# Performance work log

Hardware: AMD Instinct MI355X
Metric: run time of the kernel (lower is better)

The kernel has to match this reference:

```python
import jax, jax.numpy as jnp
import numpy as np

N_TREES = 64
DEPTH = 10           # complete binary trees
ARITY = 2
C = 8                # hidden states
M = 32               # observation labels
G = 8                # n_gen
NPT = 2 ** (DEPTH + 1) - 1   # nodes per tree = 2047
DIM = N_TREES * NPT          # 131008 total nodes


def _levels(parents_cat, children_cat):
    # Static (Python-int) slicing: level d has N_TREES * 2**d children.
    levels, pos = [], 0
    for d in range(1, DEPTH + 1):
        n = N_TREES * (2 ** d)
        levels.append((parents_cat[pos:pos + n], children_cat[pos:pos + n]))
        pos += n
    return levels


def _forward(A, B, Pi, x, roots, leaves, inv_map, trees_ind, parents_cat, children_cat):
    sm_A = jax.nn.softmax(A, axis=0)    # (C,C,G), columns sum to 1 over first axis
    sm_B = jax.nn.softmax(B, axis=1)    # (C,M,G)
    sm_Pi = jax.nn.softmax(Pi, axis=0)  # (C,G)
    log_A, log_Pi = jnp.log(sm_A), jnp.log(sm_Pi)

    levels = _levels(parents_cat, children_cat)
    obs = x[inv_map]
    emit = lambda idx: jnp.transpose(sm_B[:, obs[idx]], (1, 0, 2))  # (n,C,G)

    # ---- preliminary downward: prior[n,i,g] ----
    prior = jnp.zeros((DIM, C, G), dtype=A.dtype)
    prior = prior.at[roots].set(jnp.broadcast_to(sm_Pi, (roots.shape[0], C, G)))
    for pa, ch in levels:
        prior = prior.at[ch].set(jnp.einsum('ijg,njg->nig', sm_A, prior[pa]))

    # ---- upward (beta recursion) ----
    beta = jnp.zeros((DIM, C, G), dtype=A.dtype)
    t_beta = jnp.zeros((DIM, C, G), dtype=A.dtype)
    bl = prior[leaves] * emit(leaves)
    beta = beta.at[leaves].set(bl / bl.sum(1, keepdims=True))
    for pa, ch in reversed(levels):
        ratio = beta[ch] / prior[ch]                       # (n,C,G)
        beta_uv = jnp.einsum('ijg,nig->njg', sm_A, ratio)  # message child->parent
        t_beta = t_beta.at[ch].set(beta_uv)
        u_idx = pa[::ARITY]                                # unique parents (children are contiguous pairs)
        prod_u = beta_uv.reshape(-1, ARITY, C, G).prod(axis=1)  # segmented product over siblings
        bu = prior[u_idx] * emit(u_idx) * prod_u
        beta = beta.at[u_idx].set(bu / bu.sum(1, keepdims=True))

    # ---- downward (eps / t_eps posteriors) ----
    eps = jnp.zeros((DIM, C, G), dtype=A.dtype)
    t_eps = jnp.zeros((DIM, C, C, G), dtype=A.dtype)
    eps = eps.at[roots].set(beta[roots])
    for pa, ch in levels:
        pa_factor = eps[pa][:, None, :, :] * sm_A[None] / t_beta[ch][:, None, :, :]  # (n,C,C,G)
        ch_factor = (beta[ch] / prior[ch])[:, :, None, :]                            # (n,C,1,G)
        te = ch_factor * pa_factor
        t_eps = t_eps.at[ch].set(te)
        num = te.sum(2)
        eps = eps.at[ch].set(num / num.sum(1, keepdims=True))

    # ---- log likelihood, scattered per tree ----
    lik = jnp.zeros((DIM, G), dtype=A.dtype)
    lik = lik.at[roots].add((eps[roots] * log_Pi[None]).sum(1))
    no_root = jnp.concatenate([ch for _, ch in levels])
    lik = lik.at[no_root].add((t_eps[no_root] * log_A[None]).sum((1, 2)))
    internal = jnp.concatenate([pa[::ARITY] for pa, _ in levels])
    all_nodes = jnp.concatenate([internal, leaves])
    lik = lik.at[all_nodes].add((eps[all_nodes] * jnp.log(emit(all_nodes))).sum(1))
    ll = jax.ops.segment_sum(lik, trees_ind, num_segments=N_TREES)  # (N_TREES, G)
    return -ll


def setup_inputs() -> dict:
    key = jax.random.key(0)
    kA, kB, kPi, kx = jax.random.split(key, 4)
    A = jax.random.normal(kA, (C, C, G), dtype=jnp.float32)
    B = jax.random.normal(kB, (C, M, G), dtype=jnp.float32)
    Pi = jax.random.normal(kPi, (C, G), dtype=jnp.float32)
    x = jax.random.randint(kx, (DIM,), 0, M, dtype=jnp.int32)

    offsets = np.arange(N_TREES, dtype=np.int64) * NPT
    parents, children = [], []
    for d in range(1, DEPTH + 1):
        cl = np.arange(2 ** d - 1, 2 ** (d + 1) - 1)   # local child indices at level d
        pl = (cl - 1) // 2                             # local parent indices
        children.append((offsets[:, None] + cl[None, :]).ravel())
        parents.append((offsets[:, None] + pl[None, :]).ravel())
    parents_cat = jnp.asarray(np.concatenate(parents), dtype=jnp.int32)
    children_cat = jnp.asarray(np.concatenate(children), dtype=jnp.int32)
    leaves = jnp.asarray(children[-1], dtype=jnp.int32)
    roots = jnp.asarray(offsets, dtype=jnp.int32)
    inv_map = jnp.arange(DIM, dtype=jnp.int32)
    trees_ind = jnp.asarray(np.repeat(np.arange(N_TREES), NPT), dtype=jnp.int32)
    return {"A": A, "B": B, "Pi": Pi, "x": x, "roots": roots, "leaves": leaves,
            "inv_map": inv_map, "trees_ind": trees_ind,
            "parents_cat": parents_cat, "children_cat": children_cat}


def reference(A, B, Pi, x, roots, leaves, inv_map, trees_ind, parents_cat, children_cat):
    return _forward(A, B, Pi, x, roots, leaves, inv_map, trees_ind, parents_cat, children_cat)
```

## Files before the change

### kernel.cpp

```cpp
#include <hip/hip_runtime.h>


#define NTREES 64
#define DEPTH  10
#define C      8
#define M      32
#define G      8
#define NPT    2047
#define PAD    9
#define BLOCK  512
#define LNODES 1023

__device__ __forceinline__ float frcp(float v) { return __builtin_amdgcn_rcpf(v); }

template<bool WEPS>
__device__ __forceinline__ float child_node(const float (&sA)[C][C],
                                            const float (&sAL)[C][C],
                                            const float (&lgB)[C][M],
                                            const float (&r)[C],
                                            const float (&epa)[C],
                                            int xv,
                                            float (&eout)[C])
{
    float f[C];
    #pragma unroll
    for (int j = 0; j < C; ++j) {
        float tb = 0.f;
        #pragma unroll
        for (int i = 0; i < C; ++i) tb += sA[i][j] * r[i];
        f[j] = epa[j] * frcp(tb);
    }
    float S = 0.f, likA = 0.f, num[C];
    #pragma unroll
    for (int i = 0; i < C; ++i) {
        float a = 0.f, la = 0.f;
        #pragma unroll
        for (int j = 0; j < C; ++j) { a += sA[i][j] * f[j]; la += sAL[i][j] * f[j]; }
        num[i] = r[i] * a;
        S     += num[i];
        likA  += r[i] * la;
    }
    const float invS = frcp(S);
    float likE = 0.f;
    #pragma unroll
    for (int i = 0; i < C; ++i) {
        const float e2 = num[i] * invS;
        if constexpr (WEPS) eout[i] = e2;
        likE += e2 * lgB[i][xv];
    }
    return likA + likE;
}

__global__ __launch_bounds__(BLOCK, 2)
void htmm_kernel(const float* __restrict__ A,
                 const float* __restrict__ B,
                 const float* __restrict__ Pi,
                 const int*   __restrict__ x,
                 float* __restrict__ out)
{
    __shared__ float buf[LNODES * PAD];
    __shared__ float sA[C][C], sAL[C][C];
    __shared__ float sB[C][M], lgB[C][M];
    __shared__ float spi[C],  lgpi[C];
    __shared__ float bls[C];
    __shared__ float red8[BLOCK / 64];

    const int b   = blockIdx.x;
    const int t   = b >> 3;
    const int g   = b & 7;
    const int tid = threadIdx.x;
    const int base = t * NPT;

    if (tid < C) {
        const int j = tid;
        float w[C]; float mx = -1e30f;
        #pragma unroll
        for (int i = 0; i < C; ++i) { w[i] = A[(i*C + j)*G + g]; mx = fmaxf(mx, w[i]); }
        float s = 0.f; float e[C];
        #pragma unroll
        for (int i = 0; i < C; ++i) { e[i] = expf(w[i] - mx); s += e[i]; }
        const float inv = 1.f / s, ls = logf(s);
        #pragma unroll
        for (int i = 0; i < C; ++i) {
            const float sm = e[i] * inv;
            sA[i][j]  = sm;
            sAL[i][j] = sm * ((w[i] - mx) - ls);
        }
    } else if (tid == 8) {
        float w[C]; float mx = -1e30f;
        #pragma unroll
        for (int c = 0; c < C; ++c) { w[c] = Pi[c*G + g]; mx = fmaxf(mx, w[c]); }
        float s = 0.f; float e[C];
        #pragma unroll
        for (int c = 0; c < C; ++c) { e[c] = expf(w[c] - mx); s += e[c]; }
        const float inv = 1.f / s, ls = logf(s);
        #pragma unroll
        for (int c = 0; c < C; ++c) { spi[c] = e[c]*inv; lgpi[c] = (w[c]-mx) - ls; }
    } else if (tid >= 64 && tid < 64 + C) {
        const int c = tid - 64;
        float mx = -1e30f;
        for (int m = 0; m < M; ++m) mx = fmaxf(mx, B[(c*M + m)*G + g]);
        float s = 0.f;
        for (int m = 0; m < M; ++m) s += expf(B[(c*M + m)*G + g] - mx);
        bls[c] = mx + logf(s);
    }
    __syncthreads();

    if (tid < C * M) {
        const int c = tid >> 5, m = tid & 31;
        const float d0 = B[(c*M + m)*G + g] - bls[c];
        lgB[c][m] = d0;
        sB[c][m]  = expf(d0);
    }
    if (tid == 320) {
        #pragma unroll
        for (int i = 0; i < C; ++i) buf[i] = spi[i];
    }
    __syncthreads();

    for (int d = 1; d <= 8; ++d) {
        const int half = 1 << (d - 1);
        if (tid < half) {
            const int u = half - 1 + tid;
            const int cb = 2*u + 1;
            float p[C];
            #pragma unroll
            for (int j = 0; j < C; ++j) p[j] = buf[u*PAD + j];
            #pragma unroll
            for (int i = 0; i < C; ++i) {
                float acc = 0.f;
                #pragma unroll
                for (int j = 0; j < C; ++j) acc += sA[i][j] * p[j];
                buf[cb*PAD + i]       = acc;
                buf[(cb + 1)*PAD + i] = acc;
            }
        }
        __syncthreads();
    }

    const int s  = 511 + tid;
    const int xs = x[base + s];
    const int x1 = x[base + 2*s + 1];
    const int x2 = x[base + 2*s + 2];

    float ps[C], pc[C];
    {
        const int pas = 255 + (tid >> 1);
        float pp[C];
        #pragma unroll
        for (int j = 0; j < C; ++j) pp[j] = buf[pas*PAD + j];
        #pragma unroll
        for (int i = 0; i < C; ++i) {
            float a = 0.f;
            #pragma unroll
            for (int j = 0; j < C; ++j) a += sA[i][j] * pp[j];
            ps[i] = a;
        }
        #pragma unroll
        for (int i = 0; i < C; ++i) {
            float a = 0.f;
            #pragma unroll
            for (int j = 0; j < C; ++j) a += sA[i][j] * ps[j];
            pc[i] = a;
        }
    }

    float rs[C], r1[C], r2[C];
    {
        float Z1 = 0.f, Z2 = 0.f;
        #pragma unroll
        for (int i = 0; i < C; ++i) {
            r1[i] = sB[i][x1]; Z1 += pc[i] * r1[i];
            r2[i] = sB[i][x2]; Z2 += pc[i] * r2[i];
        }
        const float i1 = frcp(Z1), i2 = frcp(Z2);
        #pragma unroll
        for (int i = 0; i < C; ++i) { r1[i] *= i1; r2[i] *= i2; }
        float Z = 0.f;
        #pragma unroll
        for (int j = 0; j < C; ++j) {
            float a1 = 0.f, a2 = 0.f;
            #pragma unroll
            for (int i = 0; i < C; ++i) { a1 += sA[i][j]*r1[i]; a2 += sA[i][j]*r2[i]; }
            rs[j] = sB[j][xs] * (a1 * a2);
            Z += ps[j] * rs[j];
        }
        const float iz = frcp(Z);
        #pragma unroll
        for (int j = 0; j < C; ++j) { rs[j] *= iz; buf[s*PAD + j] = rs[j]; }
    }
    __syncthreads();

    for (int d = 8; d >= 0; --d) {
        if (tid < (1 << d)) {
            const int u = (1 << d) - 1 + tid;
            const int c1 = 2*u + 1;
            float rr1[C], rr2[C];
            #pragma unroll
            for (int i = 0; i < C; ++i) { rr1[i] = buf[c1*PAD + i]; rr2[i] = buf[(c1+1)*PAD + i]; }
            const int xu = x[base + u];
            float pr[C], ep[C]; float Z = 0.f;
            #pragma unroll
            for (int j = 0; j < C; ++j) {
                float a1 = 0.f, a2 = 0.f;
                #pragma unroll
                for (int i = 0; i < C; ++i) { a1 += sA[i][j]*rr1[i]; a2 += sA[i][j]*rr2[i]; }
                ep[j] = sB[j][xu] * (a1 * a2);
                pr[j] = buf[u*PAD + j];
                Z += pr[j] * ep[j];
            }
            const float iz = frcp(Z);
            if (d) {
                #pragma unroll
                for (int j = 0; j < C; ++j) buf[u*PAD + j] = ep[j]*iz;
            } else {
                #pragma unroll
                for (int j = 0; j < C; ++j) buf[j] = pr[j]*ep[j]*iz;
            }
        }
        __syncthreads();
    }

    float lik = 0.f;
    if (tid == 0) {
        const int xr = x[base];
        #pragma unroll
        for (int c = 0; c < C; ++c) lik += buf[c] * (lgpi[c] + lgB[c][xr]);
    }
    for (int d = 1; d <= 8; ++d) {
        if (tid < (1 << d)) {
            const int v = (1 << d) - 1 + tid, pa = (v - 1) >> 1;
            float epa[C], r[C], eo[C];
            #pragma unroll
            for (int j = 0; j < C; ++j) epa[j] = buf[pa*PAD + j];
            #pragma unroll
            for (int i = 0; i < C; ++i) r[i] = buf[v*PAD + i];
            lik += child_node<true>(sA, sAL, lgB, r, epa, x[base + v], eo);
            #pragma unroll
            for (int i = 0; i < C; ++i) buf[v*PAD + i] = eo[i];
        }
        __syncthreads();
    }
    {
        const int pas = 255 + (tid >> 1);
        float epa[C], es[C], dummy[C];
        #pragma unroll
        for (int j = 0; j < C; ++j) epa[j] = buf[pas*PAD + j];
        lik += child_node<true >(sA, sAL, lgB, rs, epa, xs, es);
        lik += child_node<false>(sA, sAL, lgB, r1, es,  x1, dummy);
        lik += child_node<false>(sA, sAL, lgB, r2, es,  x2, dummy);
    }

    #pragma unroll
    for (int off = 32; off; off >>= 1) lik += __shfl_xor(lik, off, 64);
    if ((tid & 63) == 0) red8[tid >> 6] = lik;
    __syncthreads();
    if (tid == 0) {
        float acc = 0.f;
        #pragma unroll
        for (int w = 0; w < BLOCK/64; ++w) acc += red8[w];
        out[t*G + g] = -acc;
    }
}

extern "C" void kernel_launch(void* const* d_in, const int* in_sizes, int n_in,
                              void* d_out, int out_size, void* d_ws, size_t ws_size,
                              hipStream_t stream) {
    const float* A  = (const float*)d_in[0];
    const float* B  = (const float*)d_in[1];
    const float* Pi = (const float*)d_in[2];
    const int*   x  = (const int*)d_in[3];
    float* out = (float*)d_out;
    htmm_kernel<<<NTREES * G, BLOCK, 0, stream>>>(A, B, Pi, x, out);
}
```

Baseline: 117.0 us.

## Process two tree levels per barrier in the down, up and posterior passes

Each thread now handles a node together with its children (or grandchildren) in one step, so the prior, beta and posterior sweeps take about half as many __syncthreads barriers. The aim is to cut the serial barrier-bound level chain in a kernel where most threads sit idle at the upper levels. The cost is redundant work per thread and more live registers. Global loads of x for the leaf frontier are also hoisted ahead of the softmax setup so their latency overlaps it.

```diff
diff --git a/kernel.cpp b/kernel.cpp
--- a/kernel.cpp
+++ b/kernel.cpp
@@ -13,6 +13,54 @@
 
 __device__ __forceinline__ float frcp(float v) { return __builtin_amdgcn_rcpf(v); }
 
+__device__ __forceinline__ void ldsRead(const float* buf, int node, float (&v)[C]) {
+    #pragma unroll
+    for (int i = 0; i < C; ++i) v[i] = buf[node*PAD + i];
+}
+__device__ __forceinline__ void ldsWrite(float* buf, int node, const float (&v)[C]) {
+    #pragma unroll
+    for (int i = 0; i < C; ++i) buf[node*PAD + i] = v[i];
+}
+
+__device__ __forceinline__ void matvec(const float (&sA)[C][C], const float (&p)[C],
+                                       float (&o)[C]) {
+    #pragma unroll
+    for (int i = 0; i < C; ++i) {
+        float a = 0.f;
+        #pragma unroll
+        for (int j = 0; j < C; ++j) a += sA[i][j] * p[j];
+        o[i] = a;
+    }
+}
+
+template<bool ROOT>
+__device__ __forceinline__ void up_node(const float (&sA)[C][C], const float (&sB)[C][M],
+                                        const float (&rr1)[C], const float (&rr2)[C],
+                                        const float (&pr)[C], int xu, float (&outv)[C])
+{
+    float a1[C], a2[C];
+    #pragma unroll
+    for (int j = 0; j < C; ++j) { a1[j] = 0.f; a2[j] = 0.f; }
+    #pragma unroll
+    for (int i = 0; i < C; ++i) {
+        #pragma unroll
+        for (int j = 0; j < C; ++j) {
+            const float aij = sA[i][j];
+            a1[j] += aij * rr1[i];
+            a2[j] += aij * rr2[i];
+        }
+    }
+    float ep[C]; float Z = 0.f;
+    #pragma unroll
+    for (int j = 0; j < C; ++j) {
+        ep[j] = sB[j][xu] * (a1[j] * a2[j]);
+        Z += pr[j] * ep[j];
+    }
+    const float iz = frcp(Z);
+    #pragma unroll
+    for (int j = 0; j < C; ++j) outv[j] = ROOT ? pr[j]*ep[j]*iz : ep[j]*iz;
+}
+
 template<bool WEPS>
 __device__ __forceinline__ float child_node(const float (&sA)[C][C],
                                             const float (&sAL)[C][C],
@@ -22,14 +70,17 @@
                                             int xv,
                                             float (&eout)[C])
 {
+    float tb[C];
+    #pragma unroll
+    for (int j = 0; j < C; ++j) tb[j] = 0.f;
+    #pragma unroll
+    for (int i = 0; i < C; ++i) {
+        #pragma unroll
+        for (int j = 0; j < C; ++j) tb[j] += sA[i][j] * r[i];
+    }
     float f[C];
     #pragma unroll
-    for (int j = 0; j < C; ++j) {
-        float tb = 0.f;
-        #pragma unroll
-        for (int i = 0; i < C; ++i) tb += sA[i][j] * r[i];
-        f[j] = epa[j] * frcp(tb);
-    }
+    for (int j = 0; j < C; ++j) f[j] = epa[j] * frcp(tb[j]);
     float S = 0.f, likA = 0.f, num[C];
     #pragma unroll
     for (int i = 0; i < C; ++i) {
@@ -71,15 +122,20 @@
     const int tid = threadIdx.x;
     const int base = t * NPT;
 
+    const int s  = 511 + tid;
+    const int xs = x[base + s];
+    const int x1 = x[base + 2*s + 1];
+    const int x2 = x[base + 2*s + 2];
+
     if (tid < C) {
         const int j = tid;
         float w[C]; float mx = -1e30f;
         #pragma unroll
         for (int i = 0; i < C; ++i) { w[i] = A[(i*C + j)*G + g]; mx = fmaxf(mx, w[i]); }
-        float s = 0.f; float e[C];
-        #pragma unroll
-        for (int i = 0; i < C; ++i) { e[i] = expf(w[i] - mx); s += e[i]; }
-        const float inv = 1.f / s, ls = logf(s);
+        float s0 = 0.f; float e[C];
+        #pragma unroll
+        for (int i = 0; i < C; ++i) { e[i] = expf(w[i] - mx); s0 += e[i]; }
+        const float inv = 1.f / s0, ls = logf(s0);
         #pragma unroll
         for (int i = 0; i < C; ++i) {
             const float sm = e[i] * inv;
@@ -90,19 +146,21 @@
         float w[C]; float mx = -1e30f;
         #pragma unroll
         for (int c = 0; c < C; ++c) { w[c] = Pi[c*G + g]; mx = fmaxf(mx, w[c]); }
-        float s = 0.f; float e[C];
-        #pragma unroll
-        for (int c = 0; c < C; ++c) { e[c] = expf(w[c] - mx); s += e[c]; }
-        const float inv = 1.f / s, ls = logf(s);
+        float s0 = 0.f; float e[C];
+        #pragma unroll
+        for (int c = 0; c < C; ++c) { e[c] = expf(w[c] - mx); s0 += e[c]; }
+        const float inv = 1.f / s0, ls = logf(s0);
         #pragma unroll
         for (int c = 0; c < C; ++c) { spi[c] = e[c]*inv; lgpi[c] = (w[c]-mx) - ls; }
     } else if (tid >= 64 && tid < 64 + C) {
         const int c = tid - 64;
         float mx = -1e30f;
+        #pragma unroll
         for (int m = 0; m < M; ++m) mx = fmaxf(mx, B[(c*M + m)*G + g]);
-        float s = 0.f;
-        for (int m = 0; m < M; ++m) s += expf(B[(c*M + m)*G + g] - mx);
-        bls[c] = mx + logf(s);
+        float s0 = 0.f;
+        #pragma unroll
+        for (int m = 0; m < M; ++m) s0 += expf(B[(c*M + m)*G + g] - mx);
+        bls[c] = mx + logf(s0);
     }
     __syncthreads();
 
@@ -118,53 +176,30 @@
     }
     __syncthreads();
 
-    for (int d = 1; d <= 8; ++d) {
-        const int half = 1 << (d - 1);
-        if (tid < half) {
-            const int u = half - 1 + tid;
-            const int cb = 2*u + 1;
-            float p[C];
-            #pragma unroll
-            for (int j = 0; j < C; ++j) p[j] = buf[u*PAD + j];
-            #pragma unroll
-            for (int i = 0; i < C; ++i) {
-                float acc = 0.f;
-                #pragma unroll
-                for (int j = 0; j < C; ++j) acc += sA[i][j] * p[j];
-                buf[cb*PAD + i]       = acc;
-                buf[(cb + 1)*PAD + i] = acc;
-            }
+    #pragma unroll 1
+    for (int p = 0; p < 8; p += 2) {
+        if (tid < (1 << p)) {
+            const int u = (1 << p) - 1 + tid;
+            float pp[C], c[C], gk[C];
+            ldsRead(buf, u, pp);
+            matvec(sA, pp, c);
+            matvec(sA, c,  gk);
+            const int cb = 2*u + 1, gb = 4*u + 3;
+            ldsWrite(buf, cb,   c);  ldsWrite(buf, cb+1, c);
+            ldsWrite(buf, gb,   gk); ldsWrite(buf, gb+1, gk);
+            ldsWrite(buf, gb+2, gk); ldsWrite(buf, gb+3, gk);
         }
         __syncthreads();
     }
-
-    const int s  = 511 + tid;
-    const int xs = x[base + s];
-    const int x1 = x[base + 2*s + 1];
-    const int x2 = x[base + 2*s + 2];
 
     float ps[C], pc[C];
     {
         const int pas = 255 + (tid >> 1);
         float pp[C];
-        #pragma unroll
-        for (int j = 0; j < C; ++j) pp[j] = buf[pas*PAD + j];
-        #pragma unroll
-        for (int i = 0; i < C; ++i) {
-            float a = 0.f;
-            #pragma unroll
-            for (int j = 0; j < C; ++j) a += sA[i][j] * pp[j];
-            ps[i] = a;
-        }
-        #pragma unroll
-        for (int i = 0; i < C; ++i) {
-            float a = 0.f;
-            #pragma unroll
-            for (int j = 0; j < C; ++j) a += sA[i][j] * ps[j];
-            pc[i] = a;
-        }
-    }
-
+        ldsRead(buf, pas, pp);
+        matvec(sA, pp, ps);
+        matvec(sA, ps, pc);
+    }
     float rs[C], r1[C], r2[C];
     {
         float Z1 = 0.f, Z2 = 0.f;
@@ -176,76 +211,79 @@
         const float i1 = frcp(Z1), i2 = frcp(Z2);
         #pragma unroll
         for (int i = 0; i < C; ++i) { r1[i] *= i1; r2[i] *= i2; }
-        float Z = 0.f;
-        #pragma unroll
-        for (int j = 0; j < C; ++j) {
-            float a1 = 0.f, a2 = 0.f;
-            #pragma unroll
-            for (int i = 0; i < C; ++i) { a1 += sA[i][j]*r1[i]; a2 += sA[i][j]*r2[i]; }
-            rs[j] = sB[j][xs] * (a1 * a2);
-            Z += ps[j] * rs[j];
-        }
-        const float iz = frcp(Z);
-        #pragma unroll
-        for (int j = 0; j < C; ++j) { rs[j] *= iz; buf[s*PAD + j] = rs[j]; }
-    }
-    __syncthreads();
-
-    for (int d = 8; d >= 0; --d) {
-        if (tid < (1 << d)) {
-            const int u = (1 << d) - 1 + tid;
-            const int c1 = 2*u + 1;
-            float rr1[C], rr2[C];
-            #pragma unroll
-            for (int i = 0; i < C; ++i) { rr1[i] = buf[c1*PAD + i]; rr2[i] = buf[(c1+1)*PAD + i]; }
-            const int xu = x[base + u];
-            float pr[C], ep[C]; float Z = 0.f;
-            #pragma unroll
-            for (int j = 0; j < C; ++j) {
-                float a1 = 0.f, a2 = 0.f;
-                #pragma unroll
-                for (int i = 0; i < C; ++i) { a1 += sA[i][j]*rr1[i]; a2 += sA[i][j]*rr2[i]; }
-                ep[j] = sB[j][xu] * (a1 * a2);
-                pr[j] = buf[u*PAD + j];
-                Z += pr[j] * ep[j];
+        up_node<false>(sA, sB, r1, r2, ps, xs, rs);
+        ldsWrite(buf, s, rs);
+    }
+    __syncthreads();
+
+    #pragma unroll 1
+    for (int p = 7; p >= 1; p -= 2) {
+        if (tid < (1 << p)) {
+            const int u  = (1 << p) - 1 + tid;
+            const int c1 = 2*u + 1, c2 = 2*u + 2;
+            float rc1[C], rc2[C];
+            {
+                float ra[C], rb[C], pr[C];
+                ldsRead(buf, 2*c1+1, ra); ldsRead(buf, 2*c1+2, rb); ldsRead(buf, c1, pr);
+                up_node<false>(sA, sB, ra, rb, pr, x[base + c1], rc1);
             }
-            const float iz = frcp(Z);
-            if (d) {
-                #pragma unroll
-                for (int j = 0; j < C; ++j) buf[u*PAD + j] = ep[j]*iz;
-            } else {
-                #pragma unroll
-                for (int j = 0; j < C; ++j) buf[j] = pr[j]*ep[j]*iz;
+            {
+                float ra[C], rb[C], pr[C];
+                ldsRead(buf, 2*c2+1, ra); ldsRead(buf, 2*c2+2, rb); ldsRead(buf, c2, pr);
+                up_node<false>(sA, sB, ra, rb, pr, x[base + c2], rc2);
             }
+            float pr[C], ru[C];
+            ldsRead(buf, u, pr);
+            up_node<false>(sA, sB, rc1, rc2, pr, x[base + u], ru);
+            ldsWrite(buf, c1, rc1); ldsWrite(buf, c2, rc2); ldsWrite(buf, u, ru);
         }
         __syncthreads();
     }
+    if (tid == 0) {
+        float ra[C], rb[C], pr[C], er[C];
+        ldsRead(buf, 1, ra); ldsRead(buf, 2, rb); ldsRead(buf, 0, pr);
+        up_node<true>(sA, sB, ra, rb, pr, x[base], er);
+        ldsWrite(buf, 0, er);
+    }
+    __syncthreads();
 
     float lik = 0.f;
     if (tid == 0) {
         const int xr = x[base];
-        #pragma unroll
-        for (int c = 0; c < C; ++c) lik += buf[c] * (lgpi[c] + lgB[c][xr]);
-    }
-    for (int d = 1; d <= 8; ++d) {
-        if (tid < (1 << d)) {
-            const int v = (1 << d) - 1 + tid, pa = (v - 1) >> 1;
-            float epa[C], r[C], eo[C];
-            #pragma unroll
-            for (int j = 0; j < C; ++j) epa[j] = buf[pa*PAD + j];
-            #pragma unroll
-            for (int i = 0; i < C; ++i) r[i] = buf[v*PAD + i];
-            lik += child_node<true>(sA, sAL, lgB, r, epa, x[base + v], eo);
-            #pragma unroll
-            for (int i = 0; i < C; ++i) buf[v*PAD + i] = eo[i];
+        float er[C];
+        ldsRead(buf, 0, er);
+        #pragma unroll
+        for (int c = 0; c < C; ++c) lik += er[c] * (lgpi[c] + lgB[c][xr]);
+    }
+    #pragma unroll 1
+    for (int q = 1; q <= 7; q += 2) {
+        if (tid < (1 << q)) {
+            const int v = (1 << q) - 1 + tid, pa = (v - 1) >> 1;
+            float epa[C], r[C], ev[C];
+            ldsRead(buf, pa, epa);
+            ldsRead(buf, v, r);
+            lik += child_node<true>(sA, sAL, lgB, r, epa, x[base + v], ev);
+            ldsWrite(buf, v, ev);
+            const int c1 = 2*v + 1;
+            {
+                float rc[C], ec[C];
+                ldsRead(buf, c1, rc);
+                lik += child_node<true>(sA, sAL, lgB, rc, ev, x[base + c1], ec);
+                ldsWrite(buf, c1, ec);
+            }
+            {
+                float rc[C], ec[C];
+                ldsRead(buf, c1+1, rc);
+                lik += child_node<true>(sA, sAL, lgB, rc, ev, x[base + c1 + 1], ec);
+                ldsWrite(buf, c1+1, ec);
+            }
         }
         __syncthreads();
     }
     {
         const int pas = 255 + (tid >> 1);
         float epa[C], es[C], dummy[C];
-        #pragma unroll
-        for (int j = 0; j < C; ++j) epa[j] = buf[pas*PAD + j];
+        ldsRead(buf, pas, epa);
         lik += child_node<true >(sA, sAL, lgB, rs, epa, xs, es);
         lik += child_node<false>(sA, sAL, lgB, r1, es,  x1, dummy);
         lik += child_node<false>(sA, sAL, lgB, r2, es,  x2, dummy);
```

After: 128.5 us. 1.1x slower.
